# Optimization experiments

Hardware: AMD Instinct MI355X
Metric: run time of the kernel (lower is better)

The kernel has to match this reference:

```python
import jax, jax.numpy as jnp
import numpy as np
from jax import lax

ROWS, COLS, HID = 5, 5, 4
N = ROWS * COLS
NUM_NEURONS = 128


def _nbr_indices(i, direction):
    # Faithful to get_neighbor_hidden, including the row-wrap behavior of
    # 'col-1'/'col+1' (no column bounds check in the original code).
    row, col = divmod(i, COLS)
    up = (row - 1) * COLS + col
    dn = (row + 1) * COLS + col
    lf = row * COLS + col - 1
    rt = row * COLS + col + 1
    return [up, dn, lf, rt] if direction == 'f' else [up, dn, rt, lf]


def _gather_neighbors(h, idxs):
    # h: (N, bs, HID); returns (bs, 4) of the 4th hidden feature per neighbor
    bs = h.shape[1]
    cols_list = [h[j][:, 3] if 0 <= j < N else jnp.zeros((bs,), h.dtype) for j in idxs]
    return jnp.stack(cols_list, axis=1)


def _make_step(Wx, Wh, Wn, b, direction):
    # One timestep: nodes updated sequentially (node i sees already-updated
    # up/left neighbors within the same timestep, matching the torch loop).
    def step(carry, x_t):  # x_t: (N, bs)
        h, c = carry  # each (N, bs, HID)
        for i in range(N):
            nb = _gather_neighbors(h, _nbr_indices(i, direction))  # (bs,4)
            gates = x_t[i][:, None] @ Wx + h[i] @ Wh + nb @ Wn + b  # (bs,4H)
            ig, fg, og, cc = jnp.split(gates, 4, axis=1)
            nc = jax.nn.sigmoid(fg) * c[i] + jax.nn.sigmoid(ig) * jnp.tanh(cc)
            nh = jax.nn.sigmoid(og) * jnp.tanh(nc)
            h = h.at[i].set(nh)
            c = c.at[i].set(nc)
        return (h, c), None
    return step


def _forward(x, h0f, c0f, h0b, c0b, Wx_f, Wh_f, Wn_f, b_f,
             Wx_b, Wh_b, Wn_b, b_b, W_ff, b_ff, W_out, b_out):
    bs = x.shape[0]
    x_seq = jnp.transpose(x, (2, 1, 0))  # (T, N, bs)
    (hf, cf), _ = lax.scan(_make_step(Wx_f, Wh_f, Wn_f, b_f, 'f'), (h0f, c0f), x_seq)
    (hb, cb), _ = lax.scan(_make_step(Wx_b, Wh_b, Wn_b, b_b, 'b'), (h0b, c0b), x_seq[::-1])
    H_fwd = jnp.transpose(hf, (1, 0, 2))  # (bs, N, HID)
    H_bwd = jnp.transpose(hb, (1, 0, 2))
    H = jnp.concatenate([H_fwd, H_bwd], axis=2).reshape(bs, -1)  # (bs, 200)
    ff = jax.nn.sigmoid(H @ W_ff + b_ff)
    return jax.nn.softmax(ff @ W_out + b_out, axis=1)


def setup_inputs() -> dict:
    key = jax.random.key(0)
    ks = jax.random.split(key, 16)
    bs, T = 8192, 128
    d = {}
    d['x'] = jax.random.normal(ks[0], (bs, N, T), jnp.float32)
    for nm, k in zip(['h0f', 'c0f', 'h0b', 'c0b'], ks[1:5]):
        d[nm] = jax.random.normal(k, (N, bs, HID), jnp.float32) * 0.01
    def lin(k, i, o):
        return jax.random.normal(k, (i, o), jnp.float32) * (1.0 / np.sqrt(i))
    d['Wx_f'] = lin(ks[5], 1, 4 * HID)
    d['Wh_f'] = lin(ks[6], HID, 4 * HID)
    d['Wn_f'] = lin(ks[7], 4, 4 * HID)
    d['b_f'] = jnp.zeros((4 * HID,), jnp.float32)
    d['Wx_b'] = lin(ks[8], 1, 4 * HID)
    d['Wh_b'] = lin(ks[9], HID, 4 * HID)
    d['Wn_b'] = lin(ks[10], 4, 4 * HID)
    d['b_b'] = jnp.zeros((4 * HID,), jnp.float32)
    d['W_ff'] = lin(ks[11], N * 2 * HID, NUM_NEURONS)
    d['b_ff'] = jnp.zeros((NUM_NEURONS,), jnp.float32)
    d['W_out'] = lin(ks[12], NUM_NEURONS, 2)
    d['b_out'] = jnp.zeros((2,), jnp.float32)
    return d


def reference(x, h0f, c0f, h0b, c0b, Wx_f, Wh_f, Wn_f, b_f,
              Wx_b, Wh_b, Wn_b, b_b, W_ff, b_ff, W_out, b_out):
    return _forward(x, h0f, c0f, h0b, c0b, Wx_f, Wh_f, Wn_f, b_f,
                    Wx_b, Wh_b, Wn_b, b_b, W_ff, b_ff, W_out, b_out)
```

## Files before the change

kernel.cpp:

```cpp
#include <hip/hip_runtime.h>
#include <stddef.h>

#define BS 8192
#define NNODE 25
#define TT 128
#define TCH 16
#define NW (TT / TCH)
#define XPAD 65
#define LOG2E 1.4426950408889634f

typedef float v2f __attribute__((ext_vector_type(2)));
typedef float v4f __attribute__((ext_vector_type(4)));

__device__ __forceinline__ float ex2(float x) { return __builtin_amdgcn_exp2f(x); }
__device__ __forceinline__ float rcp_(float x) { return __builtin_amdgcn_rcpf(x); }

__device__ float g_hf[NNODE * BS * 4];
__device__ float g_hb[NNODE * BS * 4];

template <int K>
__device__ __forceinline__ float bcast4(float v) {
  int s = __builtin_bit_cast(int, v);
  int r = __builtin_amdgcn_update_dpp(0, s, (K * 0x55), 0xF, 0xF, true);
  return __builtin_bit_cast(float, r);
}

__device__ __forceinline__ void acc2(v2f& A, v2f& B, float s, v2f wa, v2f wb) {
  v2f sv = {s, s};
  A = __builtin_elementwise_fma(sv, wa, A);
  B = __builtin_elementwise_fma(sv, wb, B);
}

template <int DIR>
__device__ __forceinline__ void rnn_run(
    int tid, const float* __restrict__ xblk, float* __restrict__ xs,
    const float* __restrict__ h0, const float* __restrict__ c0,
    const float* __restrict__ Wx, const float* __restrict__ Wh,
    const float* __restrict__ Wn, const float* __restrict__ Bb,
    float* __restrict__ ho, int b) {
  const int d = tid & 3;
  const int bl = tid >> 2;
  const int cI = d, cF = 4 + d, cO = 8 + d, cC = 12 + d;
  const float sS = -LOG2E, sC = 2.0f * LOG2E;

  v2f wA[9], wB[9];
  wA[0] = v2f{sS * Wx[cI], sS * Wx[cF]};
  wB[0] = v2f{sS * Wx[cO], sC * Wx[cC]};
#pragma unroll
  for (int k = 0; k < 4; ++k) {
    wA[1 + k] = v2f{sS * Wh[k * 16 + cI], sS * Wh[k * 16 + cF]};
    wB[1 + k] = v2f{sS * Wh[k * 16 + cO], sC * Wh[k * 16 + cC]};
  }
  const int nrow[4] = {0, 1, DIR ? 3 : 2, DIR ? 2 : 3};
#pragma unroll
  for (int k = 0; k < 4; ++k) {
    wA[5 + k] = v2f{sS * Wn[nrow[k] * 16 + cI], sS * Wn[nrow[k] * 16 + cF]};
    wB[5 + k] = v2f{sS * Wn[nrow[k] * 16 + cO], sC * Wn[nrow[k] * 16 + cC]};
  }
  const v2f bA = {sS * Bb[cI], sS * Bb[cF]};
  const v2f bB = {sS * Bb[cO], sC * Bb[cC]};

  float h[NNODE], c[NNODE], b3[NNODE];
#pragma unroll
  for (int i = 0; i < NNODE; ++i) {
    h[i] = h0[(i * BS + b) * 4 + d];
    c[i] = c0[(i * BS + b) * 4 + d];
    b3[i] = bcast4<3>(h[i]);
  }

  const int t4 = tid & 3;
  const int s0 = tid >> 2;

  for (int w = 0; w < NW; ++w) {
    __syncthreads();
#pragma unroll
    for (int r = 0; r < NNODE; ++r) {
      const int seg = s0 + 64 * r;
      const int sbl = seg / 25;
      const int sii = seg - sbl * 25;
      const int tb = (DIR ? (TT - TCH - TCH * w) : (TCH * w)) + 4 * t4;
      const v4f v = *(const v4f*)(xblk + ((size_t)sbl * NNODE + sii) * TT + tb);
#pragma unroll
      for (int j = 0; j < 4; ++j) {
        const int kk = DIR ? (15 - 4 * t4 - j) : (4 * t4 + j);
        xs[(kk * NNODE + sii) * XPAD + sbl] = v[j];
      }
    }
    __syncthreads();

#pragma unroll 1
    for (int kk = 0; kk < TCH; ++kk) {
      float xq[NNODE];
#pragma unroll
      for (int i = 0; i < NNODE; ++i) xq[i] = xs[(kk * NNODE + i) * XPAD + bl];

#pragma unroll
      for (int i = 0; i < NNODE; ++i) {
        const float f0 = bcast4<0>(h[i]);
        const float f1 = bcast4<1>(h[i]);
        const float f2 = bcast4<2>(h[i]);

        v2f A = bA, B = bB;
        acc2(A, B, xq[i], wA[0], wB[0]);
        acc2(A, B, f0, wA[1], wB[1]);
        acc2(A, B, f1, wA[2], wB[2]);
        acc2(A, B, f2, wA[3], wB[3]);
        acc2(A, B, b3[i], wA[4], wB[4]);
        if (i >= 5) acc2(A, B, b3[i - 5], wA[5], wB[5]);
        if (i < 20) acc2(A, B, b3[i + 5], wA[6], wB[6]);
        if (i >= 1) acc2(A, B, b3[i - 1], wA[7], wB[7]);
        if (i < 24) acc2(A, B, b3[i + 1], wA[8], wB[8]);

        const float Ei = ex2(A.x);
        const float Ef = ex2(A.y);
        const float Eo = ex2(B.x);
        const float Ec = ex2(B.y);
        const float Di = 1.0f + Ei;
        const float Df = 1.0f + Ef;
        const float P = Di * (Ec + 1.0f);
        const float num = fmaf(c[i], P, (Ec - 1.0f) * Df);
        const float nc = num * rcp_(Df * P);
        const float En = ex2(-2.0f * LOG2E * nc);
        const float hn = (1.0f - En) * rcp_((1.0f + En) * (1.0f + Eo));
        c[i] = nc;
        h[i] = hn;
        b3[i] = bcast4<3>(hn);
      }
    }
  }

#pragma unroll
  for (int i = 0; i < NNODE; ++i) ho[(i * BS + b) * 4 + d] = h[i];
}

__global__ __launch_bounds__(256, 1) void rnn_kernel(
    const float* __restrict__ x,
    const float* __restrict__ h0f, const float* __restrict__ c0f,
    const float* __restrict__ h0b, const float* __restrict__ c0b,
    const float* __restrict__ Wxf, const float* __restrict__ Whf,
    const float* __restrict__ Wnf, const float* __restrict__ bf,
    const float* __restrict__ Wxb, const float* __restrict__ Whb,
    const float* __restrict__ Wnb, const float* __restrict__ bb_) {
  __shared__ float xs[TCH * NNODE * XPAD];
  const int tid = threadIdx.x;
  const int b = blockIdx.x * 64 + (tid >> 2);
  const float* xblk = x + (size_t)(blockIdx.x * 64) * (NNODE * TT);
  if (blockIdx.y == 0) {
    rnn_run<0>(tid, xblk, xs, h0f, c0f, Wxf, Whf, Wnf, bf, g_hf, b);
  } else {
    rnn_run<1>(tid, xblk, xs, h0b, c0b, Wxb, Whb, Wnb, bb_, g_hb, b);
  }
}

__global__ __launch_bounds__(128) void ff_kernel(
    const float* __restrict__ Wff, const float* __restrict__ bff,
    const float* __restrict__ Wout, const float* __restrict__ bout,
    float* __restrict__ out) {
  __shared__ float Hs[8][200];
  __shared__ float ffs[8][129];
  const int tid = threadIdx.x;
  const int b0 = blockIdx.x * 8;

  for (int idx = tid; idx < 8 * 200; idx += 128) {
    const int bb = idx / 200;
    const int k = idx - bb * 200;
    const int i = k >> 3;
    const int dd = k & 7;
    const int b = b0 + bb;
    Hs[bb][k] = (dd < 4) ? g_hf[(i * BS + b) * 4 + dd]
                         : g_hb[(i * BS + b) * 4 + (dd - 4)];
  }
  __syncthreads();

  float acc[8];
  const float bv = bff[tid];
#pragma unroll
  for (int bb = 0; bb < 8; ++bb) acc[bb] = bv;
  for (int k = 0; k < 200; ++k) {
    const float w = Wff[k * 128 + tid];
#pragma unroll
    for (int bb = 0; bb < 8; ++bb) acc[bb] = fmaf(Hs[bb][k], w, acc[bb]);
  }
#pragma unroll
  for (int bb = 0; bb < 8; ++bb)
    ffs[bb][tid] = rcp_(1.0f + ex2(-LOG2E * acc[bb]));
  __syncthreads();

  if (tid < 8) {
    float z0 = bout[0], z1 = bout[1];
    for (int n = 0; n < 128; ++n) {
      const float f = ffs[tid][n];
      z0 = fmaf(f, Wout[n * 2 + 0], z0);
      z1 = fmaf(f, Wout[n * 2 + 1], z1);
    }
    const float m = fmaxf(z0, z1);
    const float e0 = ex2(LOG2E * (z0 - m)), e1 = ex2(LOG2E * (z1 - m));
    const float s = rcp_(e0 + e1);
    out[(size_t)(b0 + tid) * 2 + 0] = e0 * s;
    out[(size_t)(b0 + tid) * 2 + 1] = e1 * s;
  }
}

extern "C" void kernel_launch(void* const* d_in, const int* in_sizes, int n_in,
                              void* d_out, int out_size, void* d_ws, size_t ws_size,
                              hipStream_t stream) {
  (void)in_sizes; (void)n_in; (void)out_size; (void)d_ws; (void)ws_size;
  const float* x    = (const float*)d_in[0];
  const float* h0f  = (const float*)d_in[1];
  const float* c0f  = (const float*)d_in[2];
  const float* h0b  = (const float*)d_in[3];
  const float* c0b  = (const float*)d_in[4];
  const float* Wxf  = (const float*)d_in[5];
  const float* Whf  = (const float*)d_in[6];
  const float* Wnf  = (const float*)d_in[7];
  const float* bf   = (const float*)d_in[8];
  const float* Wxb  = (const float*)d_in[9];
  const float* Whb  = (const float*)d_in[10];
  const float* Wnb  = (const float*)d_in[11];
  const float* bb   = (const float*)d_in[12];
  const float* Wff  = (const float*)d_in[13];
  const float* bff  = (const float*)d_in[14];
  const float* Wout = (const float*)d_in[15];
  const float* bout = (const float*)d_in[16];
  float* out = (float*)d_out;

  rnn_kernel<<<dim3(128, 2), dim3(256), 0, stream>>>(
      x, h0f, c0f, h0b, c0b, Wxf, Whf, Wnf, bf, Wxb, Whb, Wnb, bb);
  ff_kernel<<<dim3(1024), dim3(128), 0, stream>>>(Wff, bff, Wout, bout, out);
}
```

Before: 576.9 us.

## Split gate computation across lane pairs to double RNN parallelism and occupancy

Each batch element is now handled by 8 lanes instead of 4, with each lane computing two gate pre-activations instead of four; the exponentials are exchanged between lane halves with a xor-4 shuffle and selected by bitmask. Blocks cover 32 elements, doubling the grid, and launch bounds allow two blocks per CU. This is meant to shorten the per-lane FMA dependency chain in the latency-bound sequential recurrence and improve latency hiding. It adds shuffle traffic, redundant nonlinearity work, and register pressure under the tighter launch bound.

After: 799.5 us. 38.6% more time.

```diff
diff --git a/kernel.cpp b/kernel.cpp
--- a/kernel.cpp
+++ b/kernel.cpp
@@ -6,7 +6,8 @@
 #define TT 128
 #define TCH 16
 #define NW (TT / TCH)
-#define XPAD 65
+#define CPB 32
+#define XPAD 33
 #define LOG2E 1.4426950408889634f
 
 typedef float v2f __attribute__((ext_vector_type(2)));
@@ -25,10 +26,18 @@
   return __builtin_bit_cast(float, r);
 }
 
-__device__ __forceinline__ void acc2(v2f& A, v2f& B, float s, v2f wa, v2f wb) {
+__device__ __forceinline__ v2f xch4(v2f v) {
+  return v2f{__shfl_xor(v.x, 4), __shfl_xor(v.y, 4)};
+}
+
+__device__ __forceinline__ float bitsel(int m, float a, float b) {
+  const int r = (__builtin_bit_cast(int, a) & m) | (__builtin_bit_cast(int, b) & ~m);
+  return __builtin_bit_cast(float, r);
+}
+
+__device__ __forceinline__ void acc1(v2f& G, float s, v2f w) {
   v2f sv = {s, s};
-  A = __builtin_elementwise_fma(sv, wa, A);
-  B = __builtin_elementwise_fma(sv, wb, B);
+  G = __builtin_elementwise_fma(sv, w, G);
 }
 
 template <int DIR>
@@ -39,26 +48,24 @@
     const float* __restrict__ Wn, const float* __restrict__ Bb,
     float* __restrict__ ho, int b) {
   const int d = tid & 3;
-  const int bl = tid >> 2;
-  const int cI = d, cF = 4 + d, cO = 8 + d, cC = 12 + d;
-  const float sS = -LOG2E, sC = 2.0f * LOG2E;
-
-  v2f wA[9], wB[9];
-  wA[0] = v2f{sS * Wx[cI], sS * Wx[cF]};
-  wB[0] = v2f{sS * Wx[cO], sC * Wx[cC]};
-#pragma unroll
-  for (int k = 0; k < 4; ++k) {
-    wA[1 + k] = v2f{sS * Wh[k * 16 + cI], sS * Wh[k * 16 + cF]};
-    wB[1 + k] = v2f{sS * Wh[k * 16 + cO], sC * Wh[k * 16 + cC]};
-  }
+  const int half = (tid >> 2) & 1;
+  const int hm = -half;
+  const int bl = tid >> 3;
+  const int col0 = half * 8 + d;
+  const int col1 = col0 + 4;
+  const float s0 = -LOG2E;
+  const float s1 = half ? (2.0f * LOG2E) : (-LOG2E);
+
+  v2f w[9];
+  w[0] = v2f{s0 * Wx[col0], s1 * Wx[col1]};
+#pragma unroll
+  for (int k = 0; k < 4; ++k)
+    w[1 + k] = v2f{s0 * Wh[k * 16 + col0], s1 * Wh[k * 16 + col1]};
   const int nrow[4] = {0, 1, DIR ? 3 : 2, DIR ? 2 : 3};
 #pragma unroll
-  for (int k = 0; k < 4; ++k) {
-    wA[5 + k] = v2f{sS * Wn[nrow[k] * 16 + cI], sS * Wn[nrow[k] * 16 + cF]};
-    wB[5 + k] = v2f{sS * Wn[nrow[k] * 16 + cO], sC * Wn[nrow[k] * 16 + cC]};
-  }
-  const v2f bA = {sS * Bb[cI], sS * Bb[cF]};
-  const v2f bB = {sS * Bb[cO], sC * Bb[cC]};
+  for (int k = 0; k < 4; ++k)
+    w[5 + k] = v2f{s0 * Wn[nrow[k] * 16 + col0], s1 * Wn[nrow[k] * 16 + col1]};
+  const v2f bv = {s0 * Bb[col0], s1 * Bb[col1]};
 
   float h[NNODE], c[NNODE], b3[NNODE];
 #pragma unroll
@@ -68,22 +75,24 @@
     b3[i] = bcast4<3>(h[i]);
   }
 
-  const int t4 = tid & 3;
-  const int s0 = tid >> 2;
-
-  for (int w = 0; w < NW; ++w) {
+  for (int w8 = 0; w8 < NW; ++w8) {
     __syncthreads();
-#pragma unroll
-    for (int r = 0; r < NNODE; ++r) {
-      const int seg = s0 + 64 * r;
-      const int sbl = seg / 25;
-      const int sii = seg - sbl * 25;
-      const int tb = (DIR ? (TT - TCH - TCH * w) : (TCH * w)) + 4 * t4;
-      const v4f v = *(const v4f*)(xblk + ((size_t)sbl * NNODE + sii) * TT + tb);
-#pragma unroll
-      for (int j = 0; j < 4; ++j) {
-        const int kk = DIR ? (15 - 4 * t4 - j) : (4 * t4 + j);
-        xs[(kk * NNODE + sii) * XPAD + sbl] = v[j];
+    const int tb_base = DIR ? (TT - TCH - TCH * w8) : (TCH * w8);
+#pragma unroll
+    for (int r = 0; r < 13; ++r) {
+      const int seg = tid + 256 * r;
+      if (seg < CPB * NNODE * 4) {
+        const int t4 = seg & 3;
+        const int rest = seg >> 2;
+        const int sbl = rest / 25;
+        const int sii = rest - sbl * 25;
+        const v4f v = *(const v4f*)(xblk + ((size_t)sbl * NNODE + sii) * TT +
+                                    tb_base + 4 * t4);
+#pragma unroll
+        for (int j = 0; j < 4; ++j) {
+          const int kk = DIR ? (15 - 4 * t4 - j) : (4 * t4 + j);
+          xs[(kk * NNODE + sii) * XPAD + sbl] = v[j];
+        }
       }
     }
     __syncthreads();
@@ -100,21 +109,23 @@
         const float f1 = bcast4<1>(h[i]);
         const float f2 = bcast4<2>(h[i]);
 
-        v2f A = bA, B = bB;
-        acc2(A, B, xq[i], wA[0], wB[0]);
-        acc2(A, B, f0, wA[1], wB[1]);
-        acc2(A, B, f1, wA[2], wB[2]);
-        acc2(A, B, f2, wA[3], wB[3]);
-        acc2(A, B, b3[i], wA[4], wB[4]);
-        if (i >= 5) acc2(A, B, b3[i - 5], wA[5], wB[5]);
-        if (i < 20) acc2(A, B, b3[i + 5], wA[6], wB[6]);
-        if (i >= 1) acc2(A, B, b3[i - 1], wA[7], wB[7]);
-        if (i < 24) acc2(A, B, b3[i + 1], wA[8], wB[8]);
-
-        const float Ei = ex2(A.x);
-        const float Ef = ex2(A.y);
-        const float Eo = ex2(B.x);
-        const float Ec = ex2(B.y);
+        v2f G = bv;
+        acc1(G, xq[i], w[0]);
+        acc1(G, f0, w[1]);
+        acc1(G, f1, w[2]);
+        acc1(G, f2, w[3]);
+        acc1(G, b3[i], w[4]);
+        if (i >= 5) acc1(G, b3[i - 5], w[5]);
+        if (i < 20) acc1(G, b3[i + 5], w[6]);
+        if (i >= 1) acc1(G, b3[i - 1], w[7]);
+        if (i < 24) acc1(G, b3[i + 1], w[8]);
+
+        const v2f Em = {ex2(G.x), ex2(G.y)};
+        const v2f Sw = xch4(Em);
+        const float Ei = bitsel(hm, Sw.x, Em.x);
+        const float Ef = bitsel(hm, Sw.y, Em.y);
+        const float Eo = bitsel(hm, Em.x, Sw.x);
+        const float Ec = bitsel(hm, Em.y, Sw.y);
         const float Di = 1.0f + Ei;
         const float Df = 1.0f + Ef;
         const float P = Di * (Ec + 1.0f);
@@ -129,11 +140,13 @@
     }
   }
 
-#pragma unroll
-  for (int i = 0; i < NNODE; ++i) ho[(i * BS + b) * 4 + d] = h[i];
-}
-
-__global__ __launch_bounds__(256, 1) void rnn_kernel(
+  if (half == 0) {
+#pragma unroll
+    for (int i = 0; i < NNODE; ++i) ho[(i * BS + b) * 4 + d] = h[i];
+  }
+}
+
+__global__ __launch_bounds__(256, 2) void rnn_kernel(
     const float* __restrict__ x,
     const float* __restrict__ h0f, const float* __restrict__ c0f,
     const float* __restrict__ h0b, const float* __restrict__ c0b,
@@ -143,8 +156,8 @@
     const float* __restrict__ Wnb, const float* __restrict__ bb_) {
   __shared__ float xs[TCH * NNODE * XPAD];
   const int tid = threadIdx.x;
-  const int b = blockIdx.x * 64 + (tid >> 2);
-  const float* xblk = x + (size_t)(blockIdx.x * 64) * (NNODE * TT);
+  const int b = blockIdx.x * CPB + (tid >> 3);
+  const float* xblk = x + (size_t)(blockIdx.x * CPB) * (NNODE * TT);
   if (blockIdx.y == 0) {
     rnn_run<0>(tid, xblk, xs, h0f, c0f, Wxf, Whf, Wnf, bf, g_hf, b);
   } else {
@@ -224,7 +237,7 @@
   const float* bout = (const float*)d_in[16];
   float* out = (float*)d_out;
 
-  rnn_kernel<<<dim3(128, 2), dim3(256), 0, stream>>>(
+  rnn_kernel<<<dim3(256, 2), dim3(256), 0, stream>>>(
       x, h0f, c0f, h0b, c0b, Wxf, Whf, Wnf, bf, Wxb, Whb, Wnb, bb);
   ff_kernel<<<dim3(1024), dim3(128), 0, stream>>>(Wff, bff, Wout, bout, out);
 }
```
